# Kernel optimization log

Hardware: AMD Instinct MI355X
Metric: run time of the kernel (lower is better)

Reference implementation:

```python
import jax, jax.numpy as jnp
import numpy as np

EMBED_DIM = 1024
NUM_HEADS = 16
HEAD_DIM = EMBED_DIM // NUM_HEADS


def setup_inputs() -> dict:
    key = jax.random.key(0)
    k_x, k_wqkv, k_bqkv, k_wp, k_bp = jax.random.split(key, 5)
    B, S, D = 2, 2048, EMBED_DIM
    bound_qkv = 1.0 / np.sqrt(D)
    bound_p = 1.0 / np.sqrt(D)
    return {
        "x": jax.random.normal(k_x, (B, S, D), dtype=jnp.float32),
        # torch nn.Linear stores weight as (out, in); keep that layout
        "w_qkv": jax.random.uniform(k_wqkv, (3 * D, D), jnp.float32, -bound_qkv, bound_qkv),
        "b_qkv": jax.random.uniform(k_bqkv, (3 * D,), jnp.float32, -bound_qkv, bound_qkv),
        "w_proj": jax.random.uniform(k_wp, (D, D), jnp.float32, -bound_p, bound_p),
        "b_proj": jax.random.uniform(k_bp, (D,), jnp.float32, -bound_p, bound_p),
    }


def reference(x, w_qkv, b_qkv, w_proj, b_proj):
    B, S, D = x.shape
    H, hd = NUM_HEADS, HEAD_DIM
    qkv = x @ w_qkv.T + b_qkv                      # [B,S,3D]
    qkv = qkv.reshape(B, S, 3, H, hd)
    qkv = jnp.transpose(qkv, (2, 0, 3, 1, 4))       # [3,B,H,S,hd]
    q, k, v = qkv[0], qkv[1], qkv[2]
    scale = 1.0 / np.sqrt(hd)
    scores = jnp.einsum('bhqd,bhkd->bhqk', q, k) * scale  # [B,H,S,S]
    attn = jax.nn.softmax(scores, axis=-1)
    out = jnp.einsum('bhqk,bhkd->bhqd', attn, v)    # [B,H,S,hd]
    out = jnp.transpose(out, (0, 2, 1, 3)).reshape(B, S, D)
    return out @ w_proj.T + b_proj
```

## Files before the change

### kernel.cpp

```cpp
#include <hip/hip_runtime.h>
#include <hip/hip_bf16.h>
#include <math.h>


typedef __bf16 bf16_t;
typedef __bf16 bf16x8 __attribute__((ext_vector_type(8)));
typedef __bf16 bf16x4v __attribute__((ext_vector_type(4)));
typedef float f32x4 __attribute__((ext_vector_type(4)));
typedef float f32x16 __attribute__((ext_vector_type(16)));

#define B_ 2
#define S_ 2048
#define D_ 1024
#define H_ 16
#define HD_ 64
#define QSCALE 0.18033688011112042f

__device__ __forceinline__ void load_lds16(const void* g, void* s) {
  __builtin_amdgcn_global_load_lds((__attribute__((address_space(1))) unsigned int*)g,
                                   (__attribute__((address_space(3))) unsigned int*)s,
                                   16, 0, 0);
}

__device__ __forceinline__ bf16_t fbf16(float x) {
  unsigned u = (__builtin_bit_cast(unsigned, x) + 0x8000u) >> 16;
  unsigned short s = (unsigned short)u;
  return __builtin_bit_cast(bf16_t, s);
}
__device__ __forceinline__ unsigned pack_bf16x2(float a, float b) {
  unsigned ua = __builtin_bit_cast(unsigned, a) + 0x8000u;
  unsigned ub = __builtin_bit_cast(unsigned, b) + 0x8000u;
  return __builtin_amdgcn_perm(ub, ua, 0x07060302u);
}

__global__ void tobf16_all(const float* __restrict__ x, const float* __restrict__ wq,
                           const float* __restrict__ wp, bf16_t* __restrict__ xb,
                           bf16_t* __restrict__ wqb, bf16_t* __restrict__ wpb) {
  int bid = blockIdx.x;
  const float* in;
  bf16_t* out;
  int base;
  if (bid < 4096) { in = x; out = xb; base = bid; }
  else if (bid < 7168) { in = wq; out = wqb; base = bid - 4096; }
  else { in = wp; out = wpb; base = bid - 7168; }
  int i = base * 256 + threadIdx.x;
  float4 v = ((const float4*)in)[i];
  uint2 o;
  o.x = pack_bf16x2(v.x, v.y);
  o.y = pack_bf16x2(v.z, v.w);
  ((uint2*)out)[i] = o;
}

template <int EPI, int BN>
__global__ __launch_bounds__(256, 2) void gemm_bt(
    const bf16_t* __restrict__ A, const bf16_t* __restrict__ Bm,
    const float* __restrict__ bias,
    bf16_t* __restrict__ qb, bf16_t* __restrict__ kb, bf16_t* __restrict__ vtb,
    float* __restrict__ outf) {
  constexpr int NI = BN / 32;
  constexpr int BUF = 8192 + BN * 64;
  __shared__ __align__(16) char smem[2 * BUF];
  const int tid = threadIdx.x;
  const int w = tid >> 6, lane = tid & 63;
  const int wm = w >> 1, wn = w & 1;
  const int quad = lane >> 4, l15 = lane & 15;
  const int m0 = blockIdx.y * 128, n0 = blockIdx.x * BN;

  auto stage = [&](int kt, int bb) {
    char* bA = smem + bb * BUF;
    char* bB = bA + 8192;
#pragma unroll
    for (int i = 0; i < 2; i++) {
      int ub = w * 128 + i * 64;
      int u = ub + lane;
      int r = u >> 2, c = (u & 3) ^ ((r >> 1) & 3);
      load_lds16(A + (size_t)(m0 + r) * 1024 + kt + c * 8, bA + (size_t)ub * 16);
    }
#pragma unroll
    for (int i = 0; i < BN / 64; i++) {
      int ub = w * (BN / 64) * 64 + i * 64;
      int u = ub + lane;
      int r = u >> 2, c = (u & 3) ^ ((r >> 1) & 3);
      load_lds16(Bm + (size_t)(n0 + r) * 1024 + kt + c * 8, bB + (size_t)ub * 16);
    }
  };

  f32x4 acc[4][NI];
#pragma unroll
  for (int mi = 0; mi < 4; mi++)
#pragma unroll
    for (int ni = 0; ni < NI; ni++) acc[mi][ni] = (f32x4){0.f, 0.f, 0.f, 0.f};

  stage(0, 0);

  for (int it = 0; it < 32; it++) {
    __syncthreads();
    if (it < 31) stage((it + 1) * 32, (it + 1) & 1);
    const bf16_t* bA = (const bf16_t*)(smem + (it & 1) * BUF);
    const bf16_t* bB = (const bf16_t*)(smem + (it & 1) * BUF + 8192);

    bf16x8 af[4], bfr[NI];
#pragma unroll
    for (int mi = 0; mi < 4; mi++) {
      int r = wm * 64 + mi * 16 + l15;
      af[mi] = *(const bf16x8*)(bA + (r * 4 + (quad ^ ((r >> 1) & 3))) * 8);
    }
#pragma unroll
    for (int ni = 0; ni < NI; ni++) {
      int r = wn * (BN / 2) + ni * 16 + l15;
      bfr[ni] = *(const bf16x8*)(bB + (r * 4 + (quad ^ ((r >> 1) & 3))) * 8);
    }
#pragma unroll
    for (int mi = 0; mi < 4; mi++)
#pragma unroll
      for (int ni = 0; ni < NI; ni++)
        acc[mi][ni] = __builtin_amdgcn_mfma_f32_16x16x32_bf16(af[mi], bfr[ni], acc[mi][ni], 0, 0, 0);
  }

#pragma unroll
  for (int mi = 0; mi < 4; mi++) {
#pragma unroll
    for (int ni = 0; ni < NI; ni++) {
      int n = n0 + wn * (BN / 2) + ni * 16 + l15;
      float bv = bias[n];
#pragma unroll
      for (int r = 0; r < 4; r++) {
        int m = m0 + wm * 64 + mi * 16 + quad * 4 + r;
        float v = acc[mi][ni][r] + bv;
        if (EPI == 0) {
          int t = n >> 10;
          int rr = n & 1023;
          int hh = rr >> 6, d = rr & 63;
          int bb = m >> 11, s = m & 2047;
          size_t bh = (size_t)(bb * H_ + hh);
          if (t == 0)
            qb[(bh * S_ + s) * HD_ + d] = fbf16(v * QSCALE);
          else if (t == 1)
            kb[(bh * S_ + s) * HD_ + d] = fbf16(v);
          else
            vtb[(bh * HD_ + d) * S_ + s] = fbf16(v);
        } else {
          outf[(size_t)m * 1024 + n] = v;
        }
      }
    }
  }
}

__global__ __launch_bounds__(128, 2) void attn(
    const bf16_t* __restrict__ qb, const bf16_t* __restrict__ kb,
    const bf16_t* __restrict__ vtb, bf16_t* __restrict__ ob) {
  __shared__ __align__(16) char smem[32768];
  const int tid = threadIdx.x, w = tid >> 6, lane = tid & 63;
  const int h2 = lane >> 5, l31 = lane & 31;
  const int xaddr = ((lane ^ 32) << 2);
  const int gid = blockIdx.x;
  const int g = gid & 7, k_ = gid >> 3;
  const int bh = g * 4 + (k_ >> 5);
  const int qt = k_ & 31;
  const int b = bh >> 4, h = bh & 15;
  const size_t base = (size_t)bh * S_ * HD_;
  const size_t vbase = (size_t)bh * HD_ * S_;
  const int q0 = qt * 64;
  const int myq = q0 + w * 32 + l31;

  bf16x8 bq[4];
#pragma unroll
  for (int ks = 0; ks < 4; ks++)
    bq[ks] = *(const bf16x8*)(qb + base + (size_t)myq * 64 + ks * 16 + h2 * 8);

  auto stage = [&](int kv0, int bb) {
    char* bK = smem + bb * 16384;
    char* bV = bK + 8192;
#pragma unroll
    for (int i = 0; i < 4; i++) {
      int ub = w * 256 + i * 64;
      int u = ub + lane;
      int r = u >> 3, c = (u & 7) ^ (r & 7);
      load_lds16(kb + base + (size_t)(kv0 + r) * 64 + c * 8, bK + (size_t)ub * 16);
      load_lds16(vtb + vbase + (size_t)r * S_ + kv0 + c * 8, bV + (size_t)ub * 16);
    }
  };

  f32x16 acc_o[2];
#pragma unroll
  for (int dt = 0; dt < 2; dt++)
#pragma unroll
    for (int i = 0; i < 16; i++) acc_o[dt][i] = 0.f;
  float l_acc = 0.f;

  stage(0, 0);
  __syncthreads();
  stage(64, 1);
  f32x16 s_cur[2];
  {
    const bf16_t* bK = (const bf16_t*)smem;
#pragma unroll
    for (int mt = 0; mt < 2; mt++)
#pragma unroll
      for (int i = 0; i < 16; i++) s_cur[mt][i] = 0.f;
#pragma unroll
    for (int ks = 0; ks < 4; ks++)
#pragma unroll
      for (int mt = 0; mt < 2; mt++) {
        int r = mt * 32 + l31, c = ks * 2 + h2;
        bf16x8 ak = *(const bf16x8*)(bK + (r * 8 + (c ^ (r & 7))) * 8);
        s_cur[mt] = __builtin_amdgcn_mfma_f32_32x32x16_bf16(ak, bq[ks], s_cur[mt], 0, 0, 0);
      }
  }

  for (int j = 0; j < 32; j++) {
    const bf16_t* bV = (const bf16_t*)(smem + (j & 1) * 16384) + 4096;
    bf16x8 av[2][4];
#pragma unroll
    for (int ks = 0; ks < 4; ks++)
#pragma unroll
      for (int dt = 0; dt < 2; dt++) {
        int r = dt * 32 + l31, c = ks * 2 + h2;
        av[dt][ks] = *(const bf16x8*)(bV + (r * 8 + (c ^ (r & 7))) * 8);
      }

    __syncthreads();
    if (j < 30) stage((j + 2) * 64, j & 1);

    f32x16 s_next[2];
    if (j < 31) {
      const bf16_t* bK1 = (const bf16_t*)(smem + ((j + 1) & 1) * 16384);
#pragma unroll
      for (int mt = 0; mt < 2; mt++)
#pragma unroll
        for (int i = 0; i < 16; i++) s_next[mt][i] = 0.f;
#pragma unroll
      for (int ks = 0; ks < 4; ks++)
#pragma unroll
        for (int mt = 0; mt < 2; mt++) {
          int r = mt * 32 + l31, c = ks * 2 + h2;
          bf16x8 ak = *(const bf16x8*)(bK1 + (r * 8 + (c ^ (r & 7))) * 8);
          s_next[mt] = __builtin_amdgcn_mfma_f32_32x32x16_bf16(ak, bq[ks], s_next[mt], 0, 0, 0);
        }
    }

    unsigned pk[2][8];
    float ls = 0.f;
#pragma unroll
    for (int mt = 0; mt < 2; mt++)
#pragma unroll
      for (int i = 0; i < 8; i++) {
        float p0 = __builtin_amdgcn_exp2f(s_cur[mt][2 * i]);
        float p1 = __builtin_amdgcn_exp2f(s_cur[mt][2 * i + 1]);
        ls += p0 + p1;
        pk[mt][i] = pack_bf16x2(p0, p1);
      }
    l_acc += ls;

    bf16x8 bp[4];
#pragma unroll
    for (int mt = 0; mt < 2; mt++)
#pragma unroll
      for (int kk = 0; kk < 2; kk++) {
        unsigned a0 = pk[mt][kk * 4 + 0], a1 = pk[mt][kk * 4 + 1];
        unsigned a2 = pk[mt][kk * 4 + 2], a3 = pk[mt][kk * 4 + 3];
        unsigned r0 = (unsigned)__builtin_amdgcn_ds_bpermute(xaddr, (int)(h2 ? a0 : a2));
        unsigned r1 = (unsigned)__builtin_amdgcn_ds_bpermute(xaddr, (int)(h2 ? a1 : a3));
        union { unsigned u[4]; bf16x8 v; } bb;
        bb.u[0] = h2 ? r0 : a0;
        bb.u[1] = h2 ? r1 : a1;
        bb.u[2] = h2 ? a2 : r0;
        bb.u[3] = h2 ? a3 : r1;
        bp[mt * 2 + kk] = bb.v;
      }

#pragma unroll
    for (int ks = 0; ks < 4; ks++)
#pragma unroll
      for (int dt = 0; dt < 2; dt++)
        acc_o[dt] = __builtin_amdgcn_mfma_f32_32x32x16_bf16(av[dt][ks], bp[ks], acc_o[dt], 0, 0, 0);

    if (j < 31) {
      s_cur[0] = s_next[0];
      s_cur[1] = s_next[1];
    }
  }

  float l_tot = l_acc + (float)__shfl_xor(l_acc, 32);
  float inv = 1.0f / l_tot;

#pragma unroll
  for (int dt = 0; dt < 2; dt++)
#pragma unroll
    for (int g4 = 0; g4 < 4; g4++) {
      uint2 o;
      o.x = pack_bf16x2(acc_o[dt][g4 * 4 + 0] * inv, acc_o[dt][g4 * 4 + 1] * inv);
      o.y = pack_bf16x2(acc_o[dt][g4 * 4 + 2] * inv, acc_o[dt][g4 * 4 + 3] * inv);
      int d = dt * 32 + g4 * 8 + h2 * 4;
      *(uint2*)(ob + ((size_t)b * S_ + myq) * D_ + h * HD_ + d) = o;
    }
}

extern "C" void kernel_launch(void* const* d_in, const int* in_sizes, int n_in,
                              void* d_out, int out_size, void* d_ws, size_t ws_size,
                              hipStream_t stream) {
  const float* x = (const float*)d_in[0];
  const float* w_qkv = (const float*)d_in[1];
  const float* b_qkv = (const float*)d_in[2];
  const float* w_proj = (const float*)d_in[3];
  const float* b_proj = (const float*)d_in[4];
  float* out = (float*)d_out;

  char* ws = (char*)d_ws;
  size_t off = 0;
  bf16_t* xb = (bf16_t*)(ws + off); off += (size_t)4096 * 1024 * 2;
  bf16_t* wqkvb = (bf16_t*)(ws + off); off += (size_t)3072 * 1024 * 2;
  bf16_t* wpb = (bf16_t*)(ws + off); off += (size_t)1024 * 1024 * 2;
  bf16_t* qb = (bf16_t*)(ws + off); off += (size_t)4096 * 1024 * 2;
  bf16_t* kb = (bf16_t*)(ws + off); off += (size_t)4096 * 1024 * 2;
  bf16_t* vtb = (bf16_t*)(ws + off); off += (size_t)4096 * 1024 * 2;
  bf16_t* ob = xb;

  tobf16_all<<<8192, 256, 0, stream>>>(x, w_qkv, w_proj, xb, wqkvb, wpb);
  gemm_bt<0, 128><<<dim3(24, 32), 256, 0, stream>>>(xb, wqkvb, b_qkv, qb, kb, vtb, nullptr);
  attn<<<1024, 128, 0, stream>>>(qb, kb, vtb, ob);
  gemm_bt<1, 64><<<dim3(16, 32), 256, 0, stream>>>(ob, wpb, b_proj, nullptr, nullptr, nullptr, out);
}
```

Measured before the change: 193.7 us.

## Split attention KV range across two wave pairs and use permlane32 swap

```diff
diff --git a/kernel.cpp b/kernel.cpp
--- a/kernel.cpp
+++ b/kernel.cpp
@@ -5,9 +5,9 @@
 
 typedef __bf16 bf16_t;
 typedef __bf16 bf16x8 __attribute__((ext_vector_type(8)));
-typedef __bf16 bf16x4v __attribute__((ext_vector_type(4)));
 typedef float f32x4 __attribute__((ext_vector_type(4)));
 typedef float f32x16 __attribute__((ext_vector_type(16)));
+typedef unsigned u32x2 __attribute__((ext_vector_type(2)));
 
 #define B_ 2
 #define S_ 2048
@@ -147,13 +147,13 @@
   }
 }
 
-__global__ __launch_bounds__(128, 2) void attn(
+__global__ __launch_bounds__(256, 4) void attn(
     const bf16_t* __restrict__ qb, const bf16_t* __restrict__ kb,
     const bf16_t* __restrict__ vtb, bf16_t* __restrict__ ob) {
   __shared__ __align__(16) char smem[32768];
   const int tid = threadIdx.x, w = tid >> 6, lane = tid & 63;
   const int h2 = lane >> 5, l31 = lane & 31;
-  const int xaddr = ((lane ^ 32) << 2);
+  const int qband = w & 1, pair = w >> 1;
   const int gid = blockIdx.x;
   const int g = gid & 7, k_ = gid >> 3;
   const int bh = g * 4 + (k_ >> 5);
@@ -162,7 +162,9 @@
   const size_t base = (size_t)bh * S_ * HD_;
   const size_t vbase = (size_t)bh * HD_ * S_;
   const int q0 = qt * 64;
-  const int myq = q0 + w * 32 + l31;
+  const int myq = q0 + qband * 32 + l31;
+  const int kvbase = pair << 10;
+  char* pbase = smem + pair * 16384;
 
   bf16x8 bq[4];
 #pragma unroll
@@ -170,15 +172,20 @@
     bq[ks] = *(const bf16x8*)(qb + base + (size_t)myq * 64 + ks * 16 + h2 * 8);
 
   auto stage = [&](int kv0, int bb) {
-    char* bK = smem + bb * 16384;
-    char* bV = bK + 8192;
-#pragma unroll
-    for (int i = 0; i < 4; i++) {
-      int ub = w * 256 + i * 64;
+    char* bK = pbase + bb * 8192;
+    char* bV = bK + 4096;
+#pragma unroll
+    for (int i = 0; i < 2; i++) {
+      int ub = qband * 64 + i * 128;
       int u = ub + lane;
-      int r = u >> 3, c = (u & 7) ^ (r & 7);
-      load_lds16(kb + base + (size_t)(kv0 + r) * 64 + c * 8, bK + (size_t)ub * 16);
-      load_lds16(vtb + vbase + (size_t)r * S_ + kv0 + c * 8, bV + (size_t)ub * 16);
+      {
+        int r = u >> 3, c = (u & 7) ^ (r & 7);
+        load_lds16(kb + base + (size_t)(kv0 + r) * 64 + c * 8, bK + (size_t)ub * 16);
+      }
+      {
+        int r = u >> 2, c = (u & 3) ^ ((r >> 1) & 3);
+        load_lds16(vtb + vbase + (size_t)r * S_ + kv0 + c * 8, bV + (size_t)ub * 16);
+      }
     }
   };
 
@@ -189,112 +196,114 @@
     for (int i = 0; i < 16; i++) acc_o[dt][i] = 0.f;
   float l_acc = 0.f;
 
-  stage(0, 0);
+  stage(kvbase, 0);
   __syncthreads();
-  stage(64, 1);
-  f32x16 s_cur[2];
+  stage(kvbase + 32, 1);
+  f32x16 s_cur;
   {
-    const bf16_t* bK = (const bf16_t*)smem;
-#pragma unroll
-    for (int mt = 0; mt < 2; mt++)
-#pragma unroll
-      for (int i = 0; i < 16; i++) s_cur[mt][i] = 0.f;
-#pragma unroll
-    for (int ks = 0; ks < 4; ks++)
-#pragma unroll
-      for (int mt = 0; mt < 2; mt++) {
-        int r = mt * 32 + l31, c = ks * 2 + h2;
-        bf16x8 ak = *(const bf16x8*)(bK + (r * 8 + (c ^ (r & 7))) * 8);
-        s_cur[mt] = __builtin_amdgcn_mfma_f32_32x32x16_bf16(ak, bq[ks], s_cur[mt], 0, 0, 0);
-      }
+    const bf16_t* bK = (const bf16_t*)pbase;
+#pragma unroll
+    for (int i = 0; i < 16; i++) s_cur[i] = 0.f;
+#pragma unroll
+    for (int ks = 0; ks < 4; ks++) {
+      int r = l31, c = ks * 2 + h2;
+      bf16x8 ak = *(const bf16x8*)(bK + (r * 8 + (c ^ (r & 7))) * 8);
+      s_cur = __builtin_amdgcn_mfma_f32_32x32x16_bf16(ak, bq[ks], s_cur, 0, 0, 0);
+    }
   }
 
   for (int j = 0; j < 32; j++) {
-    const bf16_t* bV = (const bf16_t*)(smem + (j & 1) * 16384) + 4096;
-    bf16x8 av[2][4];
-#pragma unroll
-    for (int ks = 0; ks < 4; ks++)
+    const bf16_t* bV = (const bf16_t*)(pbase + (j & 1) * 8192 + 4096);
+    bf16x8 av[2][2];
+#pragma unroll
+    for (int ks = 0; ks < 2; ks++)
 #pragma unroll
       for (int dt = 0; dt < 2; dt++) {
         int r = dt * 32 + l31, c = ks * 2 + h2;
-        av[dt][ks] = *(const bf16x8*)(bV + (r * 8 + (c ^ (r & 7))) * 8);
+        av[dt][ks] = *(const bf16x8*)(bV + (r * 4 + (c ^ ((r >> 1) & 3))) * 8);
       }
 
     __syncthreads();
-    if (j < 30) stage((j + 2) * 64, j & 1);
-
-    f32x16 s_next[2];
+    if (j < 30) stage(kvbase + (j + 2) * 32, j & 1);
+
+    f32x16 s_next;
     if (j < 31) {
-      const bf16_t* bK1 = (const bf16_t*)(smem + ((j + 1) & 1) * 16384);
-#pragma unroll
-      for (int mt = 0; mt < 2; mt++)
-#pragma unroll
-        for (int i = 0; i < 16; i++) s_next[mt][i] = 0.f;
-#pragma unroll
-      for (int ks = 0; ks < 4; ks++)
-#pragma unroll
-        for (int mt = 0; mt < 2; mt++) {
-          int r = mt * 32 + l31, c = ks * 2 + h2;
-          bf16x8 ak = *(const bf16x8*)(bK1 + (r * 8 + (c ^ (r & 7))) * 8);
-          s_next[mt] = __builtin_amdgcn_mfma_f32_32x32x16_bf16(ak, bq[ks], s_next[mt], 0, 0, 0);
-        }
-    }
-
-    unsigned pk[2][8];
+      const bf16_t* bK1 = (const bf16_t*)(pbase + ((j + 1) & 1) * 8192);
+#pragma unroll
+      for (int i = 0; i < 16; i++) s_next[i] = 0.f;
+#pragma unroll
+      for (int ks = 0; ks < 4; ks++) {
+        int r = l31, c = ks * 2 + h2;
+        bf16x8 ak = *(const bf16x8*)(bK1 + (r * 8 + (c ^ (r & 7))) * 8);
+        s_next = __builtin_amdgcn_mfma_f32_32x32x16_bf16(ak, bq[ks], s_next, 0, 0, 0);
+      }
+    }
+
+    unsigned pk[8];
     float ls = 0.f;
 #pragma unroll
-    for (int mt = 0; mt < 2; mt++)
-#pragma unroll
-      for (int i = 0; i < 8; i++) {
-        float p0 = __builtin_amdgcn_exp2f(s_cur[mt][2 * i]);
-        float p1 = __builtin_amdgcn_exp2f(s_cur[mt][2 * i + 1]);
-        ls += p0 + p1;
-        pk[mt][i] = pack_bf16x2(p0, p1);
-      }
+    for (int i = 0; i < 8; i++) {
+      float p0 = __builtin_amdgcn_exp2f(s_cur[2 * i]);
+      float p1 = __builtin_amdgcn_exp2f(s_cur[2 * i + 1]);
+      ls += p0 + p1;
+      pk[i] = pack_bf16x2(p0, p1);
+    }
     l_acc += ls;
 
-    bf16x8 bp[4];
-#pragma unroll
-    for (int mt = 0; mt < 2; mt++)
-#pragma unroll
-      for (int kk = 0; kk < 2; kk++) {
-        unsigned a0 = pk[mt][kk * 4 + 0], a1 = pk[mt][kk * 4 + 1];
-        unsigned a2 = pk[mt][kk * 4 + 2], a3 = pk[mt][kk * 4 + 3];
-        unsigned r0 = (unsigned)__builtin_amdgcn_ds_bpermute(xaddr, (int)(h2 ? a0 : a2));
-        unsigned r1 = (unsigned)__builtin_amdgcn_ds_bpermute(xaddr, (int)(h2 ? a1 : a3));
-        union { unsigned u[4]; bf16x8 v; } bb;
-        bb.u[0] = h2 ? r0 : a0;
-        bb.u[1] = h2 ? r1 : a1;
-        bb.u[2] = h2 ? a2 : r0;
-        bb.u[3] = h2 ? a3 : r1;
-        bp[mt * 2 + kk] = bb.v;
-      }
-
-#pragma unroll
-    for (int ks = 0; ks < 4; ks++)
+    bf16x8 bp[2];
+#pragma unroll
+    for (int kk = 0; kk < 2; kk++) {
+      unsigned a0 = pk[kk * 4 + 0], a1 = pk[kk * 4 + 1];
+      unsigned a2 = pk[kk * 4 + 2], a3 = pk[kk * 4 + 3];
+      u32x2 r02 = __builtin_amdgcn_permlane32_swap(a0, a2, false, false);
+      u32x2 r13 = __builtin_amdgcn_permlane32_swap(a1, a3, false, false);
+      union { unsigned u[4]; bf16x8 v; } bb;
+      bb.u[0] = r02[0];
+      bb.u[1] = r13[0];
+      bb.u[2] = r02[1];
+      bb.u[3] = r13[1];
+      bp[kk] = bb.v;
+    }
+
+#pragma unroll
+    for (int ks = 0; ks < 2; ks++)
 #pragma unroll
       for (int dt = 0; dt < 2; dt++)
         acc_o[dt] = __builtin_amdgcn_mfma_f32_32x32x16_bf16(av[dt][ks], bp[ks], acc_o[dt], 0, 0, 0);
 
-    if (j < 31) {
-      s_cur[0] = s_next[0];
-      s_cur[1] = s_next[1];
-    }
-  }
-
-  float l_tot = l_acc + (float)__shfl_xor(l_acc, 32);
-  float inv = 1.0f / l_tot;
-
-#pragma unroll
-  for (int dt = 0; dt < 2; dt++)
-#pragma unroll
-    for (int g4 = 0; g4 < 4; g4++) {
-      uint2 o;
-      o.x = pack_bf16x2(acc_o[dt][g4 * 4 + 0] * inv, acc_o[dt][g4 * 4 + 1] * inv);
-      o.y = pack_bf16x2(acc_o[dt][g4 * 4 + 2] * inv, acc_o[dt][g4 * 4 + 3] * inv);
-      int d = dt * 32 + g4 * 8 + h2 * 4;
-      *(uint2*)(ob + ((size_t)b * S_ + myq) * D_ + h * HD_ + d) = o;
-    }
+    if (j < 31) s_cur = s_next;
+  }
+
+  float l_pair = l_acc + (float)__shfl_xor(l_acc, 32);
+
+  float* red = (float*)smem;
+  const int rbase = qband * (64 * 33) + lane * 33;
+  if (pair == 1) {
+#pragma unroll
+    for (int dt = 0; dt < 2; dt++)
+#pragma unroll
+      for (int i = 0; i < 16; i++) red[rbase + dt * 16 + i] = acc_o[dt][i];
+    red[rbase + 32] = l_pair;
+  }
+  __syncthreads();
+  if (pair == 0) {
+#pragma unroll
+    for (int dt = 0; dt < 2; dt++)
+#pragma unroll
+      for (int i = 0; i < 16; i++) acc_o[dt][i] += red[rbase + dt * 16 + i];
+    float inv = 1.0f / (l_pair + red[rbase + 32]);
+
+#pragma unroll
+    for (int dt = 0; dt < 2; dt++)
+#pragma unroll
+      for (int g4 = 0; g4 < 4; g4++) {
+        uint2 o;
+        o.x = pack_bf16x2(acc_o[dt][g4 * 4 + 0] * inv, acc_o[dt][g4 * 4 + 1] * inv);
+        o.y = pack_bf16x2(acc_o[dt][g4 * 4 + 2] * inv, acc_o[dt][g4 * 4 + 3] * inv);
+        int d = dt * 32 + g4 * 8 + h2 * 4;
+        *(uint2*)(ob + ((size_t)b * S_ + myq) * D_ + h * HD_ + d) = o;
+      }
+  }
 }
 
 extern "C" void kernel_launch(void* const* d_in, const int* in_sizes, int n_in,
@@ -319,6 +328,6 @@
 
   tobf16_all<<<8192, 256, 0, stream>>>(x, w_qkv, w_proj, xb, wqkvb, wpb);
   gemm_bt<0, 128><<<dim3(24, 32), 256, 0, stream>>>(xb, wqkvb, b_qkv, qb, kb, vtb, nullptr);
-  attn<<<1024, 128, 0, stream>>>(qb, kb, vtb, ob);
+  attn<<<1024, 256, 0, stream>>>(qb, kb, vtb, ob);
   gemm_bt<1, 64><<<dim3(16, 32), 256, 0, stream>>>(ob, wpb, b_proj, nullptr, nullptr, nullptr, out);
 }
```

New measurement: 188.9 us, median of 2. 2.5% less time.
